# Optimization experiments

Measured on AMD Instinct MI355X. Metric: run time of the kernel, lower is better.

## Reference

```python
import jax, jax.numpy as jnp
import numpy as np

B, NPG, EG, F, EDIM, ESM = 32, 256, 2048, 128, 16, 1280
NN, E = B * NPG, B * EG
H, Dh = 4, 128
HD = H * Dh


def setup_inputs() -> dict:
    key = jax.random.key(0)
    ks = jax.random.split(key, 32)
    x = jax.random.normal(ks[0], (NN, F), jnp.float32)
    edge_attr = jax.random.normal(ks[1], (E, EDIM), jnp.float32)
    off = jnp.repeat(jnp.arange(B, dtype=jnp.int32) * NPG, EG)
    src = off + jax.random.randint(ks[2], (E,), 0, NPG, dtype=jnp.int32)
    dst = off + jax.random.randint(ks[3], (E,), 0, NPG, dtype=jnp.int32)
    edge_index = jnp.stack([src, dst])
    batch_index = jnp.repeat(jnp.arange(B, dtype=jnp.int32), NPG)
    esm = jax.random.normal(ks[4], (B, ESM), jnp.float32)
    g = lambda i, shp: jax.random.normal(ks[i], shp, jnp.float32) * 0.05
    return dict(
        x=x, edge_attr=edge_attr, edge_index=edge_index, batch_index=batch_index,
        esm2_embeddings=esm,
        Wq=g(5, (5, F, HD)), bq=g(6, (5, HD)), Wk=g(7, (5, F, HD)), bk=g(8, (5, HD)),
        Wv=g(9, (5, F, HD)), bv=g(10, (5, HD)), We=g(11, (5, EDIM, HD)),
        Wskip=g(12, (5, F, HD)), bskip=g(13, (5, HD)), Wbeta=g(14, (5, 3 * HD)),
        Wt=g(15, (5, HD, F)), bt=g(16, (5, F)),
        gamma=1.0 + g(17, (5, F)), beta_bn=g(18, (5, F)), rmean=g(19, (5, F)),
        rvar=0.5 + jax.random.uniform(ks[20], (5, F)),
        pw=g(21, (2, F)),
        W1=g(22, (2 * F + ESM, 512)), b1=g(23, (512,)),
        W2=g(24, (512, 256)), b2=g(25, (256,)),
        W3=g(26, (256, 10)), b3=g(27, (10,)))


def _forward(x, edge_attr, esm, Wq, bq, Wk, bk, Wv, bv, We, Wskip, bskip, Wbeta,
             Wt, bt, gamma, beta_bn, rmean, rvar, pw, W1, b1, W2, b2, W3, b3,
             src, dst, batch_index):
    scale = 1.0 / jnp.sqrt(jnp.float32(Dh))

    def conv(h, li, emask):
        # PyG TransformerConv(beta=True, edge_dim) + Linear + ReLU + BatchNorm(eval)
        q = (h @ Wq[li] + bq[li]).reshape(NN, H, Dh)
        k = (h @ Wk[li] + bk[li]).reshape(NN, H, Dh)
        v = (h @ Wv[li] + bv[li]).reshape(NN, H, Dh)
        e = (edge_attr @ We[li]).reshape(E, H, Dh)   # lin_edge, bias=False
        kj = k[src] + e                               # [E,H,Dh]
        a = jnp.einsum('ehd,ehd->eh', q[dst], kj) * scale
        a = jnp.where(emask[:, None], a, -1e30)
        m = jnp.maximum(jax.ops.segment_max(a, dst, num_segments=NN), -1e30)
        ea = jnp.exp(a - m[dst]) * emask[:, None]
        den = jax.ops.segment_sum(ea, dst, num_segments=NN)
        attn = ea / jnp.maximum(den[dst], 1e-16)      # scatter-softmax over dst
        msg = (v[src] + e) * attn[..., None]
        out = jax.ops.segment_sum(msg, dst, num_segments=NN).reshape(NN, HD)
        xr = h @ Wskip[li] + bskip[li]                # root/skip path
        bta = jax.nn.sigmoid(jnp.concatenate([out, xr, out - xr], -1) @ Wbeta[li])[:, None]
        h2 = bta * xr + (1.0 - bta) * out
        h2 = jax.nn.relu(h2 @ Wt[li] + bt[li])
        return (h2 - rmean[li]) / jnp.sqrt(rvar[li] + 1e-5) * gamma[li] + beta_bn[li]

    nmask = jnp.ones((NN,), bool)
    emask = jnp.ones((E,), bool)
    h = conv(x, 0, emask)
    k_list = [NPG // 2, NPG // 4]  # ratio=0.5 applied twice
    reps = []
    for i in range(4):
        h = conv(h, i + 1, emask)
        if i % 2 == 0:  # top_k_every_n = 2
            p = i // 2
            w = pw[p]
            s = jnp.tanh((h @ w) / jnp.linalg.norm(w))      # TopKPooling score
            s_m = jnp.where(nmask, s, -jnp.inf)
            ranks = jnp.argsort(jnp.argsort(-s_m.reshape(B, NPG), axis=1), axis=1).reshape(-1)
            keep = (ranks < k_list[p]) & nmask
            h = h * s[:, None] * keep[:, None]
            nmask = keep
            emask = emask & keep[src] & keep[dst]
            cnt = jax.ops.segment_sum(keep.astype(h.dtype), batch_index, num_segments=B)
            gmax = jax.ops.segment_max(jnp.where(keep[:, None], h, -1e30), batch_index, num_segments=B)
            gmean = jax.ops.segment_sum(h * keep[:, None], batch_index, num_segments=B) / jnp.maximum(cnt, 1.0)[:, None]
            reps.append(jnp.concatenate([gmax, gmean], 1))
    g = reps[0] + reps[1]
    g = jnp.concatenate([g, esm], 1)
    g = jax.nn.relu(g @ W1 + b1)   # dropout(p=0.8) is identity at inference
    g = jax.nn.relu(g @ W2 + b2)
    return g @ W3 + b3


def reference(x, edge_attr, edge_index, batch_index, esm2_embeddings,
              Wq, bq, Wk, bk, Wv, bv, We, Wskip, bskip, Wbeta, Wt, bt,
              gamma, beta_bn, rmean, rvar, pw, W1, b1, W2, b2, W3, b3):
    src, dst = edge_index[0], edge_index[1]
    return _forward(x, edge_attr, esm2_embeddings, Wq, bq, Wk, bk, Wv, bv, We,
                    Wskip, bskip, Wbeta, Wt, bt, gamma, beta_bn, rmean, rvar,
                    pw, W1, b1, W2, b2, W3, b3, src, dst, batch_index)
```

## Files before the change

kernel.cpp:

```cpp
#include <hip/hip_runtime.h>
#include <math.h>

#define BB 32
#define NPGC 256
#define FF 128
#define EDIMC 16
#define ESMC 1280
#define NNODE 8192
#define NEDGE 65536
#define EGC 2048
#define NH 4
#define DH 128
#define HDIM 512

typedef __attribute__((ext_vector_type(8))) short bf16x8;
typedef __attribute__((ext_vector_type(4))) float f32x4;

__device__ __forceinline__ float waveReduceSum(float v) {
#pragma unroll
    for (int o = 32; o > 0; o >>= 1) v += __shfl_down(v, o);
    return v;
}

__device__ __forceinline__ unsigned short f2b(float f) {
    unsigned u = __builtin_bit_cast(unsigned, f);
    return (unsigned short)((u + 0x7fffu + ((u >> 16) & 1u)) >> 16);
}
__device__ __forceinline__ unsigned pack2(float lo, float hi) {
    return (unsigned)f2b(lo) | ((unsigned)f2b(hi) << 16);
}
__device__ __forceinline__ float2 b2f2(unsigned u) {
    float lo = __builtin_bit_cast(float, u << 16);
    float hi = __builtin_bit_cast(float, u & 0xffff0000u);
    return make_float2(lo, hi);
}

__global__ __launch_bounds__(256) void k_setup(const int* __restrict__ dst,
                                               int* __restrict__ emask,
                                               int* __restrict__ nmask,
                                               int* __restrict__ coff,
                                               int* __restrict__ ceid) {
    __shared__ int cntS[NPGC];
    __shared__ int scanS[NPGC];
    __shared__ int offS[NPGC];
    int g = blockIdx.x, t = threadIdx.x;
    cntS[t] = 0;
    nmask[g * NPGC + t] = 1;
    __syncthreads();
    int base = g * EGC;
#pragma unroll
    for (int i = 0; i < EGC / 256; ++i) {
        int e = base + i * 256 + t;
        emask[e] = 1;
        atomicAdd(&cntS[dst[e] - g * NPGC], 1);
    }
    __syncthreads();
    scanS[t] = cntS[t];
    __syncthreads();
    for (int off = 1; off < NPGC; off <<= 1) {
        int v = scanS[t];
        if (t >= off) v += scanS[t - off];
        __syncthreads();
        scanS[t] = v;
        __syncthreads();
    }
    int excl = scanS[t] - cntS[t];
    offS[t] = excl;
    coff[g * NPGC + t] = base + excl;
    if (g == 0 && t == 0) coff[NNODE] = NEDGE;
    cntS[t] = 0;
    __syncthreads();
#pragma unroll
    for (int i = 0; i < EGC / 256; ++i) {
        int e = base + i * 256 + t;
        int d = dst[e] - g * NPGC;
        int pos = atomicAdd(&cntS[d], 1);
        ceid[base + offS[d] + pos] = e;
    }
}

__global__ void k_convert(const float* __restrict__ x, const float* __restrict__ Wq,
                          const float* __restrict__ Wk, const float* __restrict__ Wv,
                          const float* __restrict__ Wsk, const float* __restrict__ Wt,
                          const float* __restrict__ W1, const float* __restrict__ W2,
                          unsigned short* __restrict__ xb, unsigned short* __restrict__ wqb,
                          unsigned short* __restrict__ wkb, unsigned short* __restrict__ wvb,
                          unsigned short* __restrict__ wskb, unsigned short* __restrict__ wtb,
                          unsigned short* __restrict__ w1b, unsigned short* __restrict__ w2b) {
    int idx = blockIdx.x * 256 + threadIdx.x;
    if (idx < 1048576) { xb[idx] = f2b(x[idx]); return; }
    idx -= 1048576;
    if (idx < 1048576) {
        int fam = idx >> 18, local = idx & 262143;
        int li = local >> 16, rem = local & 65535;
        int n = rem >> 7, k = rem & 127;
        const float* S = (fam == 0) ? Wq : (fam == 1) ? Wk : (fam == 2) ? Wv : Wsk;
        unsigned short* D = (fam == 0) ? wqb : (fam == 1) ? wkb : (fam == 2) ? wvb : wskb;
        D[local] = f2b(S[(size_t)li * 65536 + (size_t)k * 512 + n]);
        return;
    }
    idx -= 1048576;
    if (idx < 262144) {
        int li = idx >> 16, rem = idx & 65535;
        int n = rem >> 9, k = rem & 511;
        wtb[idx] = f2b(Wt[(size_t)li * 65536 + (size_t)k * 128 + n]);
        return;
    }
    idx -= 262144;
    if (idx < 786432) {
        int n = idx / 1536, k = idx % 1536;
        w1b[idx] = f2b(W1[(size_t)k * 512 + n]);
        return;
    }
    idx -= 786432;
    {
        int n = idx >> 9, k = idx & 511;
        w2b[idx] = f2b(W2[(size_t)k * 256 + n]);
    }
}

__global__ __launch_bounds__(256) void k_qkvs_mfma(
    const unsigned short* __restrict__ hb,
    const unsigned short* __restrict__ wq, const unsigned short* __restrict__ wk,
    const unsigned short* __restrict__ wv, const unsigned short* __restrict__ wsk,
    const float* __restrict__ bq, const float* __restrict__ bk,
    const float* __restrict__ bv, const float* __restrict__ bsk,
    unsigned short* __restrict__ oq, unsigned short* __restrict__ ok,
    unsigned short* __restrict__ ov, unsigned short* __restrict__ osk) {
    const unsigned short* W;
    const float* bias;
    unsigned short* out;
    if (blockIdx.z == 0) { W = wq; bias = bq; out = oq; }
    else if (blockIdx.z == 1) { W = wk; bias = bk; out = ok; }
    else if (blockIdx.z == 2) { W = wv; bias = bv; out = ov; }
    else { W = wsk; bias = bsk; out = osk; }
    int lane = threadIdx.x & 63, wave = threadIdx.x >> 6;
    int quad = lane >> 4, m = lane & 15;
    int rowbase = blockIdx.x * 128 + (wave >> 1) * 64;
    int colbase = blockIdx.y * 128 + (wave & 1) * 64;
    f32x4 zero = {0.f, 0.f, 0.f, 0.f};
    f32x4 acc[4][4];
#pragma unroll
    for (int i = 0; i < 4; ++i)
#pragma unroll
        for (int j = 0; j < 4; ++j) acc[i][j] = zero;
#pragma unroll
    for (int ks = 0; ks < 4; ++ks) {
        int k0 = ks * 32 + quad * 8;
        bf16x8 af[4], bfr[4];
#pragma unroll
        for (int tm = 0; tm < 4; ++tm)
            af[tm] = *(const bf16x8*)(hb + (size_t)(rowbase + tm * 16 + m) * FF + k0);
#pragma unroll
        for (int tn = 0; tn < 4; ++tn)
            bfr[tn] = *(const bf16x8*)(W + (size_t)(colbase + tn * 16 + m) * FF + k0);
#pragma unroll
        for (int tm = 0; tm < 4; ++tm)
#pragma unroll
            for (int tn = 0; tn < 4; ++tn)
                acc[tm][tn] = __builtin_amdgcn_mfma_f32_16x16x32_bf16(af[tm], bfr[tn],
                                                                      acc[tm][tn], 0, 0, 0);
    }
#pragma unroll
    for (int tn = 0; tn < 4; ++tn) {
        int col = colbase + tn * 16 + m;
        float bc = bias[col];
#pragma unroll
        for (int tm = 0; tm < 4; ++tm)
#pragma unroll
            for (int r = 0; r < 4; ++r)
                out[(size_t)(rowbase + tm * 16 + quad * 4 + r) * HDIM + col] =
                    f2b(acc[tm][tn][r] + bc);
    }
}

__global__ __launch_bounds__(128) void k_out_mfma(
    const unsigned short* __restrict__ h2b, const unsigned short* __restrict__ wt,
    const float* __restrict__ bt_, const float* __restrict__ gam_,
    const float* __restrict__ bet_, const float* __restrict__ rme_,
    const float* __restrict__ rva_, float* __restrict__ hout,
    unsigned short* __restrict__ hbf) {
    int lane = threadIdx.x & 63, wave = threadIdx.x >> 6;
    int quad = lane >> 4, m = lane & 15;
    int rowbase = blockIdx.x * 32;
    int colbase = wave * 64;
    f32x4 zero = {0.f, 0.f, 0.f, 0.f};
    f32x4 acc[2][4];
#pragma unroll
    for (int i = 0; i < 2; ++i)
#pragma unroll
        for (int j = 0; j < 4; ++j) acc[i][j] = zero;
    for (int ks = 0; ks < 16; ++ks) {
        int k0 = ks * 32 + quad * 8;
        bf16x8 af[2], bfr[4];
#pragma unroll
        for (int tm = 0; tm < 2; ++tm)
            af[tm] = *(const bf16x8*)(h2b + (size_t)(rowbase + tm * 16 + m) * HDIM + k0);
#pragma unroll
        for (int tn = 0; tn < 4; ++tn)
            bfr[tn] = *(const bf16x8*)(wt + (size_t)(colbase + tn * 16 + m) * HDIM + k0);
#pragma unroll
        for (int tm = 0; tm < 2; ++tm)
#pragma unroll
            for (int tn = 0; tn < 4; ++tn)
                acc[tm][tn] = __builtin_amdgcn_mfma_f32_16x16x32_bf16(af[tm], bfr[tn],
                                                                      acc[tm][tn], 0, 0, 0);
    }
#pragma unroll
    for (int tn = 0; tn < 4; ++tn) {
        int col = colbase + tn * 16 + m;
        float bc = bt_[col];
        float sc = gam_[col] * rsqrtf(rva_[col] + 1e-5f);
        float sh = bet_[col] - rme_[col] * sc;
#pragma unroll
        for (int tm = 0; tm < 2; ++tm)
#pragma unroll
            for (int r = 0; r < 4; ++r) {
                size_t o = (size_t)(rowbase + tm * 16 + quad * 4 + r) * FF + col;
                float v = fmaxf(acc[tm][tn][r] + bc, 0.f) * sc + sh;
                hout[o] = v;
                hbf[o] = f2b(v);
            }
    }
}

__global__ __launch_bounds__(256) void k_mlp_mfma(const unsigned short* __restrict__ A,
                                                  const unsigned short* __restrict__ Wt,
                                                  float* __restrict__ cp,
                                                  int N, int K, int KS) {
    int lane = threadIdx.x & 63, wave = threadIdx.x >> 6;
    int quad = lane >> 4, m = lane & 15;
    int colbase = blockIdx.x * 256 + wave * 64;
    int kc = K / KS;
    int k0b = blockIdx.y * kc;
    f32x4 zero = {0.f, 0.f, 0.f, 0.f};
    f32x4 acc[2][4];
#pragma unroll
    for (int i = 0; i < 2; ++i)
#pragma unroll
        for (int j = 0; j < 4; ++j) acc[i][j] = zero;
    for (int ks = 0; ks < kc / 32; ++ks) {
        int k0 = k0b + ks * 32 + quad * 8;
        bf16x8 a0 = *(const bf16x8*)(A + (size_t)m * K + k0);
        bf16x8 a1 = *(const bf16x8*)(A + (size_t)(16 + m) * K + k0);
        bf16x8 bfr[4];
#pragma unroll
        for (int tn = 0; tn < 4; ++tn)
            bfr[tn] = *(const bf16x8*)(Wt + (size_t)(colbase + tn * 16 + m) * K + k0);
#pragma unroll
        for (int tn = 0; tn < 4; ++tn) {
            acc[0][tn] = __builtin_amdgcn_mfma_f32_16x16x32_bf16(a0, bfr[tn], acc[0][tn], 0, 0, 0);
            acc[1][tn] = __builtin_amdgcn_mfma_f32_16x16x32_bf16(a1, bfr[tn], acc[1][tn], 0, 0, 0);
        }
    }
#pragma unroll
    for (int tm = 0; tm < 2; ++tm)
#pragma unroll
        for (int tn = 0; tn < 4; ++tn)
#pragma unroll
            for (int r = 0; r < 4; ++r)
                cp[((size_t)blockIdx.y * 32 + tm * 16 + quad * 4 + r) * N +
                   colbase + tn * 16 + m] = acc[tm][tn][r];
}

__global__ void k_mlp_fix(const float* __restrict__ cp, const float* __restrict__ b,
                          float* __restrict__ C, unsigned short* __restrict__ Cb,
                          int MN, int N, int KS, int relu) {
    int i = blockIdx.x * 256 + threadIdx.x;
    if (i >= MN) return;
    float acc = b[i % N];
    for (int s = 0; s < KS; ++s) acc += cp[(size_t)s * MN + i];
    if (relu) acc = fmaxf(acc, 0.f);
    C[i] = acc;
    if (Cb) Cb[i] = f2b(acc);
}

__global__ void k_g1(const float* __restrict__ r0, const float* __restrict__ r1,
                     const float* __restrict__ esm, unsigned short* __restrict__ g1b) {
    int i = blockIdx.x * 256 + threadIdx.x;
    int r = i / 1536, c = i % 1536;
    float v = (c < 256) ? (r0[r * 256 + c] + r1[r * 256 + c]) : esm[(size_t)r * ESMC + c - 256];
    g1b[i] = f2b(v);
}

__global__ __launch_bounds__(256) void k_attn_wave(
    const unsigned short* __restrict__ q, const unsigned short* __restrict__ kmat,
    const unsigned short* __restrict__ vmat, const unsigned short* __restrict__ xr,
    const float* __restrict__ eattr, const float* __restrict__ We,
    const float* __restrict__ Wb,
    const int* __restrict__ src, const int* __restrict__ coff,
    const int* __restrict__ ceid, const int* __restrict__ emask,
    unsigned short* __restrict__ h2) {
    int wv = threadIdx.x >> 6, ln = threadIdx.x & 63;
    int n = blockIdx.x * 4 + wv;
    int h = ln >> 4, j = ln & 15;
    int d0i = ln * 8;
    int o0 = coff[n];
    int deg = coff[n + 1] - o0;
    if (deg > 64) deg = 64;

    uint4 qu = *(const uint4*)(q + (size_t)n * HDIM + d0i);
    float2 q0 = b2f2(qu.x), q1 = b2f2(qu.y), q2 = b2f2(qu.z), q3 = b2f2(qu.w);
    float qf[8] = {q0.x, q0.y, q1.x, q1.y, q2.x, q2.y, q3.x, q3.y};

    float qp[16];
#pragma unroll
    for (int jj = 0; jj < EDIMC; ++jj) {
        const float4* wp = (const float4*)(We + (size_t)jj * HDIM + d0i);
        float4 wa = wp[0], wb4 = wp[1];
        qp[jj] = qf[0] * wa.x + qf[1] * wa.y + qf[2] * wa.z + qf[3] * wa.w +
                 qf[4] * wb4.x + qf[5] * wb4.y + qf[6] * wb4.z + qf[7] * wb4.w;
    }
#pragma unroll
    for (int off = 1; off < 16; off <<= 1)
#pragma unroll
        for (int jj = 0; jj < EDIMC; ++jj) qp[jj] += __shfl_xor(qp[jj], off);
    float qWl = qp[j];

    int e_reg = 0, s_reg = -1;
    if (ln < deg) {
        e_reg = ceid[o0 + ln];
        s_reg = emask[e_reg] ? src[e_reg] : -1;
    }

    float sc0 = -1e30f, sc1 = -1e30f, sc2 = -1e30f, sc3 = -1e30f;
    for (int i = 0; i < deg; ++i) {
        int si = __shfl(s_reg, i);
        float pr = -1e30f;
        if (si >= 0) {
            int ei = __shfl(e_reg, i);
            uint4 ku = *(const uint4*)(kmat + (size_t)si * HDIM + d0i);
            float2 k0 = b2f2(ku.x), k1 = b2f2(ku.y), k2 = b2f2(ku.z), k3 = b2f2(ku.w);
            float p = qf[0] * k0.x + qf[1] * k0.y + qf[2] * k1.x + qf[3] * k1.y +
                      qf[4] * k2.x + qf[5] * k2.y + qf[6] * k3.x + qf[7] * k3.y;
            p = fmaf(qWl, eattr[(size_t)ei * EDIMC + j], p);
            p += __shfl_xor(p, 8);
            p += __shfl_xor(p, 4);
            p += __shfl_xor(p, 2);
            p += __shfl_xor(p, 1);
            pr = p * 0.088388347648318447f;
        }
        float t0 = __shfl(pr, 0), t1 = __shfl(pr, 16);
        float t2 = __shfl(pr, 32), t3 = __shfl(pr, 48);
        if (ln == i) { sc0 = t0; sc1 = t1; sc2 = t2; sc3 = t3; }
    }

    bool valid = (ln < deg) && (s_reg >= 0);
    if (!valid) { sc0 = sc1 = sc2 = sc3 = -1e30f; }
    float m0 = sc0, m1 = sc1, m2 = sc2, m3 = sc3;
#pragma unroll
    for (int o = 32; o > 0; o >>= 1) {
        m0 = fmaxf(m0, __shfl_xor(m0, o));
        m1 = fmaxf(m1, __shfl_xor(m1, o));
        m2 = fmaxf(m2, __shfl_xor(m2, o));
        m3 = fmaxf(m3, __shfl_xor(m3, o));
    }
    float a0 = valid ? expf(sc0 - m0) : 0.f;
    float a1 = valid ? expf(sc1 - m1) : 0.f;
    float a2 = valid ? expf(sc2 - m2) : 0.f;
    float a3 = valid ? expf(sc3 - m3) : 0.f;
    float de0 = a0, de1 = a1, de2 = a2, de3 = a3;
#pragma unroll
    for (int o = 32; o > 0; o >>= 1) {
        de0 += __shfl_xor(de0, o);
        de1 += __shfl_xor(de1, o);
        de2 += __shfl_xor(de2, o);
        de3 += __shfl_xor(de3, o);
    }
    a0 /= fmaxf(de0, 1e-16f);
    a1 /= fmaxf(de1, 1e-16f);
    a2 /= fmaxf(de2, 1e-16f);
    a3 /= fmaxf(de3, 1e-16f);

    float z = 0.f;
    float out[8] = {0.f, 0.f, 0.f, 0.f, 0.f, 0.f, 0.f, 0.f};
    for (int i = 0; i < deg; ++i) {
        int si = __shfl(s_reg, i);
        if (si < 0) continue;
        float t0 = __shfl(a0, i), t1 = __shfl(a1, i);
        float t2 = __shfl(a2, i), t3 = __shfl(a3, i);
        float at = (h == 0) ? t0 : (h == 1) ? t1 : (h == 2) ? t2 : t3;
        int ei = __shfl(e_reg, i);
        z = fmaf(at, eattr[(size_t)ei * EDIMC + j], z);
        uint4 vu = *(const uint4*)(vmat + (size_t)si * HDIM + d0i);
        float2 v0 = b2f2(vu.x), v1 = b2f2(vu.y), v2 = b2f2(vu.z), v3 = b2f2(vu.w);
        out[0] = fmaf(at, v0.x, out[0]);
        out[1] = fmaf(at, v0.y, out[1]);
        out[2] = fmaf(at, v1.x, out[2]);
        out[3] = fmaf(at, v1.y, out[3]);
        out[4] = fmaf(at, v2.x, out[4]);
        out[5] = fmaf(at, v2.y, out[5]);
        out[6] = fmaf(at, v3.x, out[6]);
        out[7] = fmaf(at, v3.y, out[7]);
    }

#pragma unroll
    for (int jj = 0; jj < EDIMC; ++jj) {
        float zjj = __shfl(z, h * 16 + jj);
        const float4* wp = (const float4*)(We + (size_t)jj * HDIM + d0i);
        float4 wa = wp[0], wb4 = wp[1];
        out[0] = fmaf(zjj, wa.x, out[0]);
        out[1] = fmaf(zjj, wa.y, out[1]);
        out[2] = fmaf(zjj, wa.z, out[2]);
        out[3] = fmaf(zjj, wa.w, out[3]);
        out[4] = fmaf(zjj, wb4.x, out[4]);
        out[5] = fmaf(zjj, wb4.y, out[5]);
        out[6] = fmaf(zjj, wb4.z, out[6]);
        out[7] = fmaf(zjj, wb4.w, out[7]);
    }

    uint4 xu = *(const uint4*)(xr + (size_t)n * HDIM + d0i);
    float2 x0 = b2f2(xu.x), x1 = b2f2(xu.y), x2 = b2f2(xu.z), x3 = b2f2(xu.w);
    float xf[8] = {x0.x, x0.y, x1.x, x1.y, x2.x, x2.y, x3.x, x3.y};
    const float4* w0p = (const float4*)(Wb + d0i);
    const float4* w1p = (const float4*)(Wb + HDIM + d0i);
    const float4* w2p = (const float4*)(Wb + 2 * HDIM + d0i);
    float4 wa0 = w0p[0], wa1 = w0p[1];
    float4 wb0 = w1p[0], wb1 = w1p[1];
    float4 wc0 = w2p[0], wc1 = w2p[1];
    float w0f[8] = {wa0.x, wa0.y, wa0.z, wa0.w, wa1.x, wa1.y, wa1.z, wa1.w};
    float w1f[8] = {wb0.x, wb0.y, wb0.z, wb0.w, wb1.x, wb1.y, wb1.z, wb1.w};
    float w2f[8] = {wc0.x, wc0.y, wc0.z, wc0.w, wc1.x, wc1.y, wc1.z, wc1.w};
    float part = 0.f;
#pragma unroll
    for (int d = 0; d < 8; ++d)
        part += out[d] * w0f[d] + xf[d] * w1f[d] + (out[d] - xf[d]) * w2f[d];
#pragma unroll
    for (int o = 32; o > 0; o >>= 1) part += __shfl_xor(part, o);
    float bg = 1.f / (1.f + expf(-part));
    uint4 res;
    res.x = pack2(bg * xf[0] + (1.f - bg) * out[0], bg * xf[1] + (1.f - bg) * out[1]);
    res.y = pack2(bg * xf[2] + (1.f - bg) * out[2], bg * xf[3] + (1.f - bg) * out[3]);
    res.z = pack2(bg * xf[4] + (1.f - bg) * out[4], bg * xf[5] + (1.f - bg) * out[5]);
    res.w = pack2(bg * xf[6] + (1.f - bg) * out[6], bg * xf[7] + (1.f - bg) * out[7]);
    *(uint4*)(h2 + (size_t)n * HDIM + d0i) = res;
}

__global__ __launch_bounds__(256) void k_pool_rank(const float* __restrict__ pwv,
                                                   const float* __restrict__ h,
                                                   int* __restrict__ nmask,
                                                   int* __restrict__ emask,
                                                   const int* __restrict__ src,
                                                   const int* __restrict__ dst,
                                                   float* __restrict__ fbuf, int kc) {
    __shared__ float smS[NPGC];
    __shared__ int keepS[NPGC];
    int g = blockIdx.x, t = threadIdx.x;
    int n = g * NPGC + t;
    const float* hr = h + (size_t)n * FF;
    float nw2 = 0.f, dv = 0.f;
#pragma unroll
    for (int i = 0; i < FF; i += 4) {
        float4 wv = *(const float4*)(pwv + i);
        float4 hv = *(const float4*)(hr + i);
        nw2 += wv.x * wv.x + wv.y * wv.y + wv.z * wv.z + wv.w * wv.w;
        dv += hv.x * wv.x + hv.y * wv.y + hv.z * wv.z + hv.w * wv.w;
    }
    float s = tanhf(dv / sqrtf(nw2));
    int old = nmask[n];
    smS[t] = old ? s : -INFINITY;
    __syncthreads();
    float mys = smS[t];
    int rank = 0;
    for (int j = 0; j < NPGC; ++j) {
        float o = smS[j];
        rank += (o > mys) || (o == mys && j < t);
    }
    int kp = (rank < kc) && old;
    keepS[t] = kp;
    nmask[n] = kp;
    fbuf[n] = s * (float)kp;
    __syncthreads();
    if (emask) {
        int base = g * EGC;
        for (int ee = t; ee < EGC; ee += 256) {
            int e = base + ee;
            emask[e] = emask[e] && keepS[src[e] - g * NPGC] && keepS[dst[e] - g * NPGC];
        }
    }
}

__global__ __launch_bounds__(256) void k_pool_apply(const float* __restrict__ h,
                                                    unsigned short* __restrict__ hbf,
                                                    const float* __restrict__ fbuf,
                                                    const int* __restrict__ nmask,
                                                    float* __restrict__ pmax,
                                                    float* __restrict__ psum, int emit) {
    __shared__ float mS[4][128];
    __shared__ float sS[4][128];
    int g = blockIdx.x, seg = blockIdx.y, t = threadIdx.x;
    int l = t & 63, quar = t >> 6;
    int d2 = l * 2;
    int nbase = g * NPGC + seg * 64 + quar * 16;
    float mx0 = -1e30f, mx1 = -1e30f, sm0 = 0.f, sm1 = 0.f;
#pragma unroll 4
    for (int i = 0; i < 16; ++i) {
        int n = nbase + i;
        float f = fbuf[n];
        int kp = nmask[n];
        float2 hv = *(const float2*)(h + (size_t)n * FF + d2);
        float v0 = hv.x * f, v1 = hv.y * f;
        if (emit) *(unsigned*)(hbf + (size_t)n * FF + d2) = pack2(v0, v1);
        if (kp) {
            mx0 = fmaxf(mx0, v0);
            mx1 = fmaxf(mx1, v1);
            sm0 += v0;
            sm1 += v1;
        }
    }
    mS[quar][d2] = mx0;
    mS[quar][d2 + 1] = mx1;
    sS[quar][d2] = sm0;
    sS[quar][d2 + 1] = sm1;
    __syncthreads();
    if (t < 128) {
        float m = fmaxf(fmaxf(mS[0][t], mS[1][t]), fmaxf(mS[2][t], mS[3][t]));
        float s = sS[0][t] + sS[1][t] + sS[2][t] + sS[3][t];
        pmax[((size_t)g * 4 + seg) * 128 + t] = m;
        psum[((size_t)g * 4 + seg) * 128 + t] = s;
    }
}

__global__ void k_pool_final(const float* __restrict__ pmax, const float* __restrict__ psum,
                             float* __restrict__ rep, float invk) {
    int idx = blockIdx.x * 256 + threadIdx.x;
    if (idx >= BB * 128) return;
    int g = idx >> 7, d = idx & 127;
    float m = -1e30f, s = 0.f;
#pragma unroll
    for (int q = 0; q < 4; ++q) {
        m = fmaxf(m, pmax[((size_t)g * 4 + q) * 128 + d]);
        s += psum[((size_t)g * 4 + q) * 128 + d];
    }
    rep[(size_t)g * 256 + d] = m;
    rep[(size_t)g * 256 + 128 + d] = s * invk;
}

__global__ __launch_bounds__(256) void k_mlp_wave(const float* __restrict__ A,
                                                  const float* __restrict__ W,
                                                  const float* __restrict__ b,
                                                  float* __restrict__ C,
                                                  int M, int N, int K, int relu) {
    int wid = (blockIdx.x * 256 + threadIdx.x) >> 6;
    int lane = threadIdx.x & 63;
    if (wid >= M * N) return;
    int r = wid / N, c = wid % N;
    const float* Arow = A + (size_t)r * K;
    float acc = 0.f;
    for (int kk = lane; kk < K; kk += 64)
        acc = fmaf(Arow[kk], W[(size_t)kk * N + c], acc);
    acc = waveReduceSum(acc);
    if (lane == 0) {
        acc += b[c];
        C[wid] = relu ? fmaxf(acc, 0.f) : acc;
    }
}

extern "C" void kernel_launch(void* const* d_in, const int* in_sizes, int n_in,
                              void* d_out, int out_size, void* d_ws, size_t ws_size,
                              hipStream_t stream) {
    const float* x = (const float*)d_in[0];
    const float* eattr = (const float*)d_in[1];
    const int* eidx = (const int*)d_in[2];
    const float* esm = (const float*)d_in[4];
    const float* Wq = (const float*)d_in[5];
    const float* bq = (const float*)d_in[6];
    const float* Wk = (const float*)d_in[7];
    const float* bk = (const float*)d_in[8];
    const float* Wv = (const float*)d_in[9];
    const float* bv = (const float*)d_in[10];
    const float* We = (const float*)d_in[11];
    const float* Wsk = (const float*)d_in[12];
    const float* bsk = (const float*)d_in[13];
    const float* Wbe = (const float*)d_in[14];
    const float* Wt = (const float*)d_in[15];
    const float* bt = (const float*)d_in[16];
    const float* gam = (const float*)d_in[17];
    const float* bet = (const float*)d_in[18];
    const float* rme = (const float*)d_in[19];
    const float* rva = (const float*)d_in[20];
    const float* pw = (const float*)d_in[21];
    const float* W1 = (const float*)d_in[22];
    const float* b1 = (const float*)d_in[23];
    const float* W2 = (const float*)d_in[24];
    const float* b2 = (const float*)d_in[25];
    const float* W3 = (const float*)d_in[26];
    const float* b3 = (const float*)d_in[27];
    const int* srcp = eidx;
    const int* dstp = eidx + NEDGE;

    char* p = (char*)d_ws;
    auto alloc = [&](size_t bytes) -> void* {
        void* r = (void*)p;
        p += (bytes + 255) & ~(size_t)255;
        return r;
    };
    float* hA = (float*)alloc((size_t)NNODE * FF * 4);
    float* hB = (float*)alloc((size_t)NNODE * FF * 4);
    float* fbuf = (float*)alloc((size_t)NNODE * 4);
    float* pmax = (float*)alloc((size_t)BB * 4 * 128 * 4);
    float* psum = (float*)alloc((size_t)BB * 4 * 128 * 4);
    float* rep0 = (float*)alloc((size_t)BB * 256 * 4);
    float* rep1 = (float*)alloc((size_t)BB * 256 * 4);
    float* g2 = (float*)alloc((size_t)BB * 512 * 4);
    float* g3 = (float*)alloc((size_t)BB * 256 * 4);
    float* cp = (float*)alloc((size_t)8 * 32 * 512 * 4);
    int* nmask = (int*)alloc((size_t)NNODE * 4);
    int* emask = (int*)alloc((size_t)NEDGE * 4);
    int* coff = (int*)alloc((size_t)(NNODE + 1) * 4);
    int* ceid = (int*)alloc((size_t)NEDGE * 4);
    unsigned short* xb = (unsigned short*)alloc((size_t)NNODE * FF * 2);
    unsigned short* hbf = (unsigned short*)alloc((size_t)NNODE * FF * 2);
    unsigned short* qb16 = (unsigned short*)alloc((size_t)NNODE * HDIM * 2);
    unsigned short* kb16 = (unsigned short*)alloc((size_t)NNODE * HDIM * 2);
    unsigned short* vb16 = (unsigned short*)alloc((size_t)NNODE * HDIM * 2);
    unsigned short* xrb16 = (unsigned short*)alloc((size_t)NNODE * HDIM * 2);
    unsigned short* h2b16 = (unsigned short*)alloc((size_t)NNODE * HDIM * 2);
    unsigned short* wqb = (unsigned short*)alloc((size_t)4 * 65536 * 2);
    unsigned short* wkb = (unsigned short*)alloc((size_t)4 * 65536 * 2);
    unsigned short* wvb = (unsigned short*)alloc((size_t)4 * 65536 * 2);
    unsigned short* wskb = (unsigned short*)alloc((size_t)4 * 65536 * 2);
    unsigned short* wtb = (unsigned short*)alloc((size_t)4 * 65536 * 2);
    unsigned short* w1b = (unsigned short*)alloc((size_t)786432 * 2);
    unsigned short* w2b = (unsigned short*)alloc((size_t)131072 * 2);
    unsigned short* g1b = (unsigned short*)alloc((size_t)BB * 1536 * 2);
    unsigned short* g2b = (unsigned short*)alloc((size_t)BB * 512 * 2);

    k_setup<<<BB, 256, 0, stream>>>(dstp, emask, nmask, coff, ceid);
    k_convert<<<12800, 256, 0, stream>>>(x, Wq, Wk, Wv, Wsk, Wt, W1, W2,
                                         xb, wqb, wkb, wvb, wskb, wtb, w1b, w2b);

    auto conv = [&](int li, const unsigned short* hin_b, float* hout) {
        dim3 gq(NNODE / 128, HDIM / 128, 4);
        k_qkvs_mfma<<<gq, 256, 0, stream>>>(
            hin_b, wqb + (size_t)li * 65536, wkb + (size_t)li * 65536,
            wvb + (size_t)li * 65536, wskb + (size_t)li * 65536,
            bq + li * HDIM, bk + li * HDIM, bv + li * HDIM, bsk + li * HDIM,
            qb16, kb16, vb16, xrb16);
        const float* WeL = We + (size_t)li * EDIMC * HDIM;
        k_attn_wave<<<NNODE / 4, 256, 0, stream>>>(qb16, kb16, vb16, xrb16, eattr, WeL,
                                                   Wbe + (size_t)li * 3 * HDIM,
                                                   srcp, coff, ceid, emask, h2b16);
        k_out_mfma<<<NNODE / 32, 128, 0, stream>>>(
            h2b16, wtb + (size_t)li * 65536, bt + li * FF, gam + li * FF,
            bet + li * FF, rme + li * FF, rva + li * FF, hout, hbf);
    };

    auto pool = [&](int pi, const float* h, float* rep, int kc, bool updE, int emit) {
        k_pool_rank<<<BB, 256, 0, stream>>>(pw + pi * FF, h, nmask,
                                            updE ? emask : nullptr, srcp, dstp, fbuf, kc);
        k_pool_apply<<<dim3(BB, 4), 256, 0, stream>>>(h, hbf, fbuf, nmask, pmax, psum, emit);
        k_pool_final<<<16, 256, 0, stream>>>(pmax, psum, rep, 1.f / (float)kc);
    };

    conv(0, xb, hA);
    conv(1, hbf, hB);
    pool(0, hB, rep0, NPGC / 2, true, 1);
    conv(2, hbf, hA);
    conv(3, hbf, hB);
    pool(1, hB, rep1, NPGC / 4, false, 0);

    k_g1<<<BB * 1536 / 256, 256, 0, stream>>>(rep0, rep1, esm, g1b);
    k_mlp_mfma<<<dim3(2, 8), 256, 0, stream>>>(g1b, w1b, cp, 512, 1536, 8);
    k_mlp_fix<<<BB * 512 / 256, 256, 0, stream>>>(cp, b1, g2, g2b, BB * 512, 512, 8, 1);
    k_mlp_mfma<<<dim3(1, 8), 256, 0, stream>>>(g2b, w2b, cp, 256, 512, 8);
    k_mlp_fix<<<BB * 256 / 256, 256, 0, stream>>>(cp, b2, g3, nullptr, BB * 256, 256, 8, 1);
    k_mlp_wave<<<(BB * 10 * 64 + 255) / 256, 256, 0, stream>>>(g3, W3, b3, (float*)d_out,
                                                               BB, 10, 256, 0);
}
```

Baseline: 524.1 us.

## Merge setup into convert, fold pool_final into g1, remap blocks per XCD

Merges the CSR setup kernel into the bf16 conversion kernel as extra blocks, and folds the pool-final reduction into k_g1, which removes three kernel launches. It also remaps block indices in the QKV GEMM, attention and output kernels so that consecutive blocks (round-robined across the 8 XCDs) cover the rows of one graph, aiming to improve L2 locality for the per-graph gathers. The remapping assumes a fixed graph size and block count, and the mean divisors (128, 64) are now hardcoded in k_g1.

```diff
diff --git a/kernel.cpp b/kernel.cpp
--- a/kernel.cpp
+++ b/kernel.cpp
@@ -35,58 +35,57 @@
     return make_float2(lo, hi);
 }
 
-__global__ __launch_bounds__(256) void k_setup(const int* __restrict__ dst,
-                                               int* __restrict__ emask,
-                                               int* __restrict__ nmask,
-                                               int* __restrict__ coff,
-                                               int* __restrict__ ceid) {
+__global__ __launch_bounds__(256) void k_convert_setup(
+    const float* __restrict__ x, const float* __restrict__ Wq,
+    const float* __restrict__ Wk, const float* __restrict__ Wv,
+    const float* __restrict__ Wsk, const float* __restrict__ Wt,
+    const float* __restrict__ W1, const float* __restrict__ W2,
+    unsigned short* __restrict__ xb, unsigned short* __restrict__ wqb,
+    unsigned short* __restrict__ wkb, unsigned short* __restrict__ wvb,
+    unsigned short* __restrict__ wskb, unsigned short* __restrict__ wtb,
+    unsigned short* __restrict__ w1b, unsigned short* __restrict__ w2b,
+    const int* __restrict__ dst, int* __restrict__ emask, int* __restrict__ nmask,
+    int* __restrict__ coff, int* __restrict__ ceid) {
     __shared__ int cntS[NPGC];
     __shared__ int scanS[NPGC];
     __shared__ int offS[NPGC];
-    int g = blockIdx.x, t = threadIdx.x;
-    cntS[t] = 0;
-    nmask[g * NPGC + t] = 1;
-    __syncthreads();
-    int base = g * EGC;
-#pragma unroll
-    for (int i = 0; i < EGC / 256; ++i) {
-        int e = base + i * 256 + t;
-        emask[e] = 1;
-        atomicAdd(&cntS[dst[e] - g * NPGC], 1);
-    }
-    __syncthreads();
-    scanS[t] = cntS[t];
-    __syncthreads();
-    for (int off = 1; off < NPGC; off <<= 1) {
-        int v = scanS[t];
-        if (t >= off) v += scanS[t - off];
+    if (blockIdx.x >= 12800) {
+        int g = blockIdx.x - 12800, t = threadIdx.x;
+        cntS[t] = 0;
+        nmask[g * NPGC + t] = 1;
         __syncthreads();
-        scanS[t] = v;
+        int base = g * EGC;
+#pragma unroll
+        for (int i = 0; i < EGC / 256; ++i) {
+            int e = base + i * 256 + t;
+            emask[e] = 1;
+            atomicAdd(&cntS[dst[e] - g * NPGC], 1);
+        }
         __syncthreads();
-    }
-    int excl = scanS[t] - cntS[t];
-    offS[t] = excl;
-    coff[g * NPGC + t] = base + excl;
-    if (g == 0 && t == 0) coff[NNODE] = NEDGE;
-    cntS[t] = 0;
-    __syncthreads();
-#pragma unroll
-    for (int i = 0; i < EGC / 256; ++i) {
-        int e = base + i * 256 + t;
-        int d = dst[e] - g * NPGC;
-        int pos = atomicAdd(&cntS[d], 1);
-        ceid[base + offS[d] + pos] = e;
-    }
-}
-
-__global__ void k_convert(const float* __restrict__ x, const float* __restrict__ Wq,
-                          const float* __restrict__ Wk, const float* __restrict__ Wv,
-                          const float* __restrict__ Wsk, const float* __restrict__ Wt,
-                          const float* __restrict__ W1, const float* __restrict__ W2,
-                          unsigned short* __restrict__ xb, unsigned short* __restrict__ wqb,
-                          unsigned short* __restrict__ wkb, unsigned short* __restrict__ wvb,
-                          unsigned short* __restrict__ wskb, unsigned short* __restrict__ wtb,
-                          unsigned short* __restrict__ w1b, unsigned short* __restrict__ w2b) {
+        scanS[t] = cntS[t];
+        __syncthreads();
+        for (int off = 1; off < NPGC; off <<= 1) {
+            int v = scanS[t];
+            if (t >= off) v += scanS[t - off];
+            __syncthreads();
+            scanS[t] = v;
+            __syncthreads();
+        }
+        int excl = scanS[t] - cntS[t];
+        offS[t] = excl;
+        coff[g * NPGC + t] = base + excl;
+        if (g == 0 && t == 0) coff[NNODE] = NEDGE;
+        cntS[t] = 0;
+        __syncthreads();
+#pragma unroll
+        for (int i = 0; i < EGC / 256; ++i) {
+            int e = base + i * 256 + t;
+            int d = dst[e] - g * NPGC;
+            int pos = atomicAdd(&cntS[d], 1);
+            ceid[base + offS[d] + pos] = e;
+        }
+        return;
+    }
     int idx = blockIdx.x * 256 + threadIdx.x;
     if (idx < 1048576) { xb[idx] = f2b(x[idx]); return; }
     idx -= 1048576;
@@ -136,7 +135,10 @@
     else { W = wsk; bias = bsk; out = osk; }
     int lane = threadIdx.x & 63, wave = threadIdx.x >> 6;
     int quad = lane >> 4, m = lane & 15;
-    int rowbase = blockIdx.x * 128 + (wave >> 1) * 64;
+    int xcdx = blockIdx.x;
+    int g = (xcdx & 7) + 8 * ((xcdx >> 3) & 3);
+    int half = xcdx >> 5;
+    int rowbase = g * NPGC + half * 128 + (wave >> 1) * 64;
     int colbase = blockIdx.y * 128 + (wave & 1) * 64;
     f32x4 zero = {0.f, 0.f, 0.f, 0.f};
     f32x4 acc[4][4];
@@ -182,7 +184,10 @@
     unsigned short* __restrict__ hbf) {
     int lane = threadIdx.x & 63, wave = threadIdx.x >> 6;
     int quad = lane >> 4, m = lane & 15;
-    int rowbase = blockIdx.x * 32;
+    int bi = blockIdx.x;
+    int g = (bi & 7) + 8 * ((bi >> 3) & 3);
+    int sub = bi >> 5;
+    int rowbase = g * NPGC + sub * 32;
     int colbase = wave * 64;
     f32x4 zero = {0.f, 0.f, 0.f, 0.f};
     f32x4 acc[2][4];
@@ -275,11 +280,32 @@
     if (Cb) Cb[i] = f2b(acc);
 }
 
-__global__ void k_g1(const float* __restrict__ r0, const float* __restrict__ r1,
+__global__ void k_g1(const float* __restrict__ pmax0, const float* __restrict__ psum0,
+                     const float* __restrict__ pmax1, const float* __restrict__ psum1,
                      const float* __restrict__ esm, unsigned short* __restrict__ g1b) {
     int i = blockIdx.x * 256 + threadIdx.x;
     int r = i / 1536, c = i % 1536;
-    float v = (c < 256) ? (r0[r * 256 + c] + r1[r * 256 + c]) : esm[(size_t)r * ESMC + c - 256];
+    float v;
+    if (c < 128) {
+        float m0 = -1e30f, m1 = -1e30f;
+#pragma unroll
+        for (int q = 0; q < 4; ++q) {
+            m0 = fmaxf(m0, pmax0[((size_t)r * 4 + q) * 128 + c]);
+            m1 = fmaxf(m1, pmax1[((size_t)r * 4 + q) * 128 + c]);
+        }
+        v = m0 + m1;
+    } else if (c < 256) {
+        int d = c - 128;
+        float s0 = 0.f, s1 = 0.f;
+#pragma unroll
+        for (int q = 0; q < 4; ++q) {
+            s0 += psum0[((size_t)r * 4 + q) * 128 + d];
+            s1 += psum1[((size_t)r * 4 + q) * 128 + d];
+        }
+        v = s0 * (1.f / 128.f) + s1 * (1.f / 64.f);
+    } else {
+        v = esm[(size_t)r * ESMC + c - 256];
+    }
     g1b[i] = f2b(v);
 }
 
@@ -292,7 +318,10 @@
     const int* __restrict__ ceid, const int* __restrict__ emask,
     unsigned short* __restrict__ h2) {
     int wv = threadIdx.x >> 6, ln = threadIdx.x & 63;
-    int n = blockIdx.x * 4 + wv;
+    int bi = blockIdx.x;
+    int g = (bi & 7) + 8 * ((bi >> 3) & 3);
+    int sub = bi >> 5;
+    int n = g * NPGC + sub * 4 + wv;
     int h = ln >> 4, j = ln & 15;
     int d0i = ln * 8;
     int o0 = coff[n];
@@ -519,21 +548,6 @@
         pmax[((size_t)g * 4 + seg) * 128 + t] = m;
         psum[((size_t)g * 4 + seg) * 128 + t] = s;
     }
-}
-
-__global__ void k_pool_final(const float* __restrict__ pmax, const float* __restrict__ psum,
-                             float* __restrict__ rep, float invk) {
-    int idx = blockIdx.x * 256 + threadIdx.x;
-    if (idx >= BB * 128) return;
-    int g = idx >> 7, d = idx & 127;
-    float m = -1e30f, s = 0.f;
-#pragma unroll
-    for (int q = 0; q < 4; ++q) {
-        m = fmaxf(m, pmax[((size_t)g * 4 + q) * 128 + d]);
-        s += psum[((size_t)g * 4 + q) * 128 + d];
-    }
-    rep[(size_t)g * 256 + d] = m;
-    rep[(size_t)g * 256 + 128 + d] = s * invk;
 }
 
 __global__ __launch_bounds__(256) void k_mlp_wave(const float* __restrict__ A,
@@ -598,10 +612,10 @@
     float* hA = (float*)alloc((size_t)NNODE * FF * 4);
     float* hB = (float*)alloc((size_t)NNODE * FF * 4);
     float* fbuf = (float*)alloc((size_t)NNODE * 4);
-    float* pmax = (float*)alloc((size_t)BB * 4 * 128 * 4);
-    float* psum = (float*)alloc((size_t)BB * 4 * 128 * 4);
-    float* rep0 = (float*)alloc((size_t)BB * 256 * 4);
-    float* rep1 = (float*)alloc((size_t)BB * 256 * 4);
+    float* pmax0 = (float*)alloc((size_t)BB * 4 * 128 * 4);
+    float* psum0 = (float*)alloc((size_t)BB * 4 * 128 * 4);
+    float* pmax1 = (float*)alloc((size_t)BB * 4 * 128 * 4);
+    float* psum1 = (float*)alloc((size_t)BB * 4 * 128 * 4);
     float* g2 = (float*)alloc((size_t)BB * 512 * 4);
     float* g3 = (float*)alloc((size_t)BB * 256 * 4);
     float* cp = (float*)alloc((size_t)8 * 32 * 512 * 4);
@@ -626,12 +640,12 @@
     unsigned short* g1b = (unsigned short*)alloc((size_t)BB * 1536 * 2);
     unsigned short* g2b = (unsigned short*)alloc((size_t)BB * 512 * 2);
 
-    k_setup<<<BB, 256, 0, stream>>>(dstp, emask, nmask, coff, ceid);
-    k_convert<<<12800, 256, 0, stream>>>(x, Wq, Wk, Wv, Wsk, Wt, W1, W2,
-                                         xb, wqb, wkb, wvb, wskb, wtb, w1b, w2b);
+    k_convert_setup<<<12832, 256, 0, stream>>>(x, Wq, Wk, Wv, Wsk, Wt, W1, W2,
+                                               xb, wqb, wkb, wvb, wskb, wtb, w1b, w2b,
+                                               dstp, emask, nmask, coff, ceid);
 
     auto conv = [&](int li, const unsigned short* hin_b, float* hout) {
-        dim3 gq(NNODE / 128, HDIM / 128, 4);
+        dim3 gq(64, 4, 4);
         k_qkvs_mfma<<<gq, 256, 0, stream>>>(
             hin_b, wqb + (size_t)li * 65536, wkb + (size_t)li * 65536,
             wvb + (size_t)li * 65536, wskb + (size_t)li * 65536,
@@ -646,21 +660,21 @@
             bet + li * FF, rme + li * FF, rva + li * FF, hout, hbf);
     };
 
-    auto pool = [&](int pi, const float* h, float* rep, int kc, bool updE, int emit) {
+    auto pool = [&](int pi, const float* h, float* pmax, float* psum, int kc, bool updE,
+                    int emit) {
         k_pool_rank<<<BB, 256, 0, stream>>>(pw + pi * FF, h, nmask,
                                             updE ? emask : nullptr, srcp, dstp, fbuf, kc);
         k_pool_apply<<<dim3(BB, 4), 256, 0, stream>>>(h, hbf, fbuf, nmask, pmax, psum, emit);
-        k_pool_final<<<16, 256, 0, stream>>>(pmax, psum, rep, 1.f / (float)kc);
     };
 
     conv(0, xb, hA);
     conv(1, hbf, hB);
-    pool(0, hB, rep0, NPGC / 2, true, 1);
+    pool(0, hB, pmax0, psum0, NPGC / 2, true, 1);
     conv(2, hbf, hA);
     conv(3, hbf, hB);
-    pool(1, hB, rep1, NPGC / 4, false, 0);
-
-    k_g1<<<BB * 1536 / 256, 256, 0, stream>>>(rep0, rep1, esm, g1b);
+    pool(1, hB, pmax1, psum1, NPGC / 4, false, 0);
+
+    k_g1<<<BB * 1536 / 256, 256, 0, stream>>>(pmax0, psum0, pmax1, psum1, esm, g1b);
     k_mlp_mfma<<<dim3(2, 8), 256, 0, stream>>>(g1b, w1b, cp, 512, 1536, 8);
     k_mlp_fix<<<BB * 512 / 256, 256, 0, stream>>>(cp, b1, g2, g2b, BB * 512, 512, 8, 1);
     k_mlp_mfma<<<dim3(1, 8), 256, 0, stream>>>(g2b, w2b, cp, 256, 512, 8);
```

After: 505.9 us. 3.5% less time.
